# Kernel optimization log

Hardware: AMD Instinct MI355X
Metric: run time of the kernel (lower is better)

Reference implementation:

```python
import jax, jax.numpy as jnp
import numpy as np

NUM_ENTITIES = 100000
NUM_RELATIONS = 8
HIDDEN = 128
N_NODES = 100000
N_EDGES = 500000


def setup_inputs() -> dict:
    key = jax.random.key(0)
    ks = jax.random.split(key, 10)
    scale = 1.0 / np.sqrt(HIDDEN)
    inp = {
        "x_ids": jax.random.randint(ks[0], (N_NODES,), 0, NUM_ENTITIES),
        "edge_index": jax.random.randint(ks[1], (2, N_EDGES), 0, N_NODES),
        "edge_type": jax.random.randint(ks[2], (N_EDGES,), 0, NUM_RELATIONS),
        "emb": jax.random.normal(ks[3], (NUM_ENTITIES, HIDDEN), jnp.float32),
        "W1": jax.random.normal(ks[4], (NUM_RELATIONS, HIDDEN, HIDDEN), jnp.float32) * scale,
        "root1": jax.random.normal(ks[5], (HIDDEN, HIDDEN), jnp.float32) * scale,
        "b1": jnp.zeros((HIDDEN,), jnp.float32),
        "W2": jax.random.normal(ks[6], (NUM_RELATIONS, HIDDEN, HIDDEN), jnp.float32) * scale,
        "root2": jax.random.normal(ks[7], (HIDDEN, HIDDEN), jnp.float32) * scale,
        "b2": jnp.zeros((HIDDEN,), jnp.float32),
    }
    return inp


def rgcn_conv(x, edge_index, edge_type, W, root, bias):
    # x: [N, d]; W: [R, d, d]; PyG RGCNConv with aggr='mean' (per-relation mean)
    N, d = x.shape
    R = W.shape[0]
    src, dst = edge_index[0], edge_index[1]
    # transform every node under every relation: [N, R, d]
    h = jnp.einsum('nd,rdf->nrf', x, W)
    msg = h[src, edge_type]                       # [E, d] gather per edge
    seg = dst * R + edge_type                     # composite (node, relation) segment id
    sums = jax.ops.segment_sum(msg, seg, num_segments=N * R)
    cnt = jax.ops.segment_sum(jnp.ones((msg.shape[0], 1), x.dtype), seg, num_segments=N * R)
    agg = (sums / jnp.maximum(cnt, 1.0)).reshape(N, R, d).sum(axis=1)
    return agg + x @ root + bias


def reference(x_ids, edge_index, edge_type, emb, W1, root1, b1, W2, root2, b2):
    x = emb[x_ids]                                # embedding lookup [N, d]
    x = rgcn_conv(x, edge_index, edge_type, W1, root1, b1)
    x = jax.nn.relu(x)
    x = rgcn_conv(x, edge_index, edge_type, W2, root2, b2)
    return jax.nn.sigmoid(x)
```

## Files before the change

### kernel.cpp

```cpp
#include <hip/hip_runtime.h>

#define HD 128
#define RNUM 8
#define SCAN_BS 2048

typedef __attribute__((ext_vector_type(8))) short short8;
typedef __attribute__((ext_vector_type(4))) float float4e;

__device__ __forceinline__ unsigned short f2bf(float f) {
    unsigned int u = __float_as_uint(f);
    u += 0x7fffu + ((u >> 16) & 1u);
    return (unsigned short)(u >> 16);
}

__device__ __forceinline__ unsigned int pk2(float lo, float hi) {
    return (unsigned int)f2bf(lo) | ((unsigned int)f2bf(hi) << 16);
}

__device__ __forceinline__ void acc2(float4e& a, unsigned int u, int i) {
    a[i]     += __uint_as_float(u << 16);
    a[i + 1] += __uint_as_float(u & 0xffff0000u);
}

__device__ __forceinline__ void gload_lds16(const void* g, void* l) {
    __builtin_amdgcn_global_load_lds(
        (const __attribute__((address_space(1))) void*)g,
        (__attribute__((address_space(3))) void*)l, 16, 0, 0);
}

__global__ void zero_i(int* __restrict__ p, int n) {
    int g = blockIdx.x * blockDim.x + threadIdx.x;
    if (g < n) p[g] = 0;
}

__global__ void prep_kernel(const float* __restrict__ W1, const float* __restrict__ r1,
                            const float* __restrict__ W2, const float* __restrict__ r2,
                            unsigned short* __restrict__ WT,
                            const float* __restrict__ emb, unsigned short* __restrict__ emb16,
                            long long n8) {
    long long g = (long long)blockIdx.x * blockDim.x + threadIdx.x;
    if (g < 18 * 16384) {
        int gi = (int)g;
        int mat = gi >> 14;
        int idx = gi & 16383;
        int d = idx >> 7;
        int f = idx & 127;
        const float* src;
        int m;
        if (mat < 8)       { src = W1; m = mat; }
        else if (mat == 8) { src = r1; m = 0; }
        else if (mat < 17) { src = W2; m = mat - 9; }
        else               { src = r2; m = 0; }
        WT[mat * 16384 + f * 128 + d] = f2bf(src[(size_t)m * 16384 + d * 128 + f]);
    }
    long long h = g - 18 * 16384;
    if (h >= 0 && h < n8) {
        const float4* p = (const float4*)(emb + h * 8);
        float4 v0 = p[0], v1 = p[1];
        uint4 o;
        o.x = pk2(v0.x, v0.y);
        o.y = pk2(v0.z, v0.w);
        o.z = pk2(v1.x, v1.y);
        o.w = pk2(v1.z, v1.w);
        *(uint4*)(emb16 + h * 8) = o;
    }
}

__global__ void count_kernel(const int* __restrict__ ei, const int* __restrict__ et,
                             int* __restrict__ cnt, int E, int N) {
    int e = blockIdx.x * blockDim.x + threadIdx.x;
    if (e < E) atomicAdd(&cnt[ei[E + e] * RNUM + et[e]], 1);
}

__global__ void scan1(const int* __restrict__ in, int* __restrict__ out,
                      int* __restrict__ bsum, int n) {
    __shared__ int s[256];
    const int tid = threadIdx.x;
    const int base = blockIdx.x * SCAN_BS + tid * 8;
    int v[8];
    int sum = 0;
#pragma unroll
    for (int j = 0; j < 8; j++) {
        int x = (base + j < n) ? in[base + j] : 0;
        v[j] = sum;
        sum += x;
    }
    s[tid] = sum;
    __syncthreads();
    for (int off = 1; off < 256; off <<= 1) {
        int tv = (tid >= off) ? s[tid - off] : 0;
        __syncthreads();
        if (tid >= off) s[tid] += tv;
        __syncthreads();
    }
    int excl = (tid > 0) ? s[tid - 1] : 0;
    if (tid == 255) bsum[blockIdx.x] = s[255];
#pragma unroll
    for (int j = 0; j < 8; j++)
        if (base + j < n) out[base + j] = v[j] + excl;
}

__global__ void scan2(int* __restrict__ bsum, int nb) {
    __shared__ int s[512];
    const int tid = threadIdx.x;
    s[tid] = (tid < nb) ? bsum[tid] : 0;
    __syncthreads();
    for (int off = 1; off < 512; off <<= 1) {
        int tv = (tid >= off) ? s[tid - off] : 0;
        __syncthreads();
        if (tid >= off) s[tid] += tv;
        __syncthreads();
    }
    if (tid < nb) bsum[tid] = (tid > 0) ? s[tid - 1] : 0;
}

__global__ void scan3(int* __restrict__ out, int* __restrict__ cur,
                      const int* __restrict__ bsum, int n) {
    const int base = blockIdx.x * SCAN_BS + threadIdx.x * 8;
    const int add = bsum[blockIdx.x];
#pragma unroll
    for (int j = 0; j < 8; j++) {
        int i = base + j;
        if (i < n) {
            int v = out[i] + add;
            out[i] = v;
            cur[i] = v;
        }
    }
}

__global__ void fill_kernel(const int* __restrict__ ei, const int* __restrict__ et,
                            const int* __restrict__ ids,
                            int* __restrict__ cur, int* __restrict__ col,
                            int* __restrict__ colE, int* __restrict__ row_start,
                            int E, int N) {
    int e = blockIdx.x * blockDim.x + threadIdx.x;
    if (e == 0) row_start[RNUM * N] = E;
    if (e < E) {
        int src = ei[e];
        int pos = atomicAdd(&cur[ei[E + e] * RNUM + et[e]], 1);
        col[pos] = src;
        colE[pos] = ids[src];
    }
}

template <bool HAS_IDX, int ACT>
__launch_bounds__(256, 3)
__global__ void rgcn_fused(const int* __restrict__ row_start, const int* __restrict__ col,
                           const int* __restrict__ ids,
                           const unsigned short* __restrict__ x16,
                           const unsigned short* __restrict__ WT,
                           const float* __restrict__ bias,
                           void* __restrict__ CoutV, int N, int E) {
    __shared__ unsigned short As[64 * 128];
    __shared__ unsigned short Ws[128 * 128];

    const int tid = threadIdx.x;
    const int block0 = blockIdx.x * 64;
    const int w = tid >> 6;
    const int lane = tid & 63;
    const int ln15 = lane & 15;
    const int quad = lane >> 4;
    const int rowbase = (w & 1) * 32;
    const int colbase = (w >> 1) * 64;
    const int grp = tid >> 2;
    const int sub4 = tid & 3;
    const int mydst = block0 + grp;
    const bool rowok = (mydst < N);

    float4e acc[2][4];
#pragma unroll
    for (int i = 0; i < 2; i++)
#pragma unroll
        for (int j = 0; j < 4; j++)
#pragma unroll
            for (int q = 0; q < 4; q++) acc[i][j][q] = 0.0f;

#pragma unroll 1
    for (int s = 0; s < RNUM; s++) {
        {
            const unsigned short* Wsrc = WT + s * 16384;
#pragma unroll
            for (int i = 0; i < 8; i++) {
                int c = i * 256 + tid;
                int f = c >> 4;
                int cc = c & 15;
                const void* src = (const void*)(Wsrc + f * 128 + ((cc ^ (f & 15)) << 3));
                int cbase = i * 256 + (tid & ~63);
                gload_lds16(src, (char*)Ws + (size_t)cbase * 16);
            }
        }
        {
            float4e a[8];
#pragma unroll
            for (int j = 0; j < 8; j++) a[j] = (float4e){0.f, 0.f, 0.f, 0.f};
            int s0 = 0, s1 = 0;
            if (rowok) {
                s0 = row_start[mydst * 8 + s];
                s1 = row_start[mydst * 8 + s + 1];
            }
            const float inv = (s1 > s0) ? 1.0f / (float)(s1 - s0) : 0.0f;
            for (int e = s0; e < s1; e++) {
                int c = col[e];
                const uint4* xp = (const uint4*)(x16 + (size_t)c * HD + sub4 * 32);
                uint4 v0 = xp[0], v1 = xp[1], v2 = xp[2], v3 = xp[3];
                acc2(a[0], v0.x, 0); acc2(a[0], v0.y, 2);
                acc2(a[1], v0.z, 0); acc2(a[1], v0.w, 2);
                acc2(a[2], v1.x, 0); acc2(a[2], v1.y, 2);
                acc2(a[3], v1.z, 0); acc2(a[3], v1.w, 2);
                acc2(a[4], v2.x, 0); acc2(a[4], v2.y, 2);
                acc2(a[5], v2.z, 0); acc2(a[5], v2.w, 2);
                acc2(a[6], v3.x, 0); acc2(a[6], v3.y, 2);
                acc2(a[7], v3.z, 0); acc2(a[7], v3.w, 2);
            }
#pragma unroll
            for (int j = 0; j < 8; j++) a[j] *= inv;
#pragma unroll
            for (int j = 0; j < 4; j++) {
                uint4 o;
                o.x = pk2(a[2 * j][0], a[2 * j][1]);
                o.y = pk2(a[2 * j][2], a[2 * j][3]);
                o.z = pk2(a[2 * j + 1][0], a[2 * j + 1][1]);
                o.w = pk2(a[2 * j + 1][2], a[2 * j + 1][3]);
                int ck = sub4 * 4 + j;
                *(uint4*)&As[grp * 128 + ((ck ^ (grp & 15)) << 3)] = o;
            }
        }
        __syncthreads();

#pragma unroll
        for (int k0 = 0; k0 < 4; k0++) {
            short8 af[2], bf[4];
            const int ck = k0 * 4 + quad;
#pragma unroll
            for (int rt = 0; rt < 2; rt++) {
                int m = rowbase + rt * 16 + ln15;
                af[rt] = *(const short8*)&As[m * 128 + ((ck ^ (m & 15)) << 3)];
            }
#pragma unroll
            for (int ct = 0; ct < 4; ct++) {
                int n = colbase + ct * 16 + ln15;
                bf[ct] = *(const short8*)&Ws[n * 128 + ((ck ^ (n & 15)) << 3)];
            }
#pragma unroll
            for (int rt = 0; rt < 2; rt++)
#pragma unroll
                for (int ct = 0; ct < 4; ct++)
                    acc[rt][ct] = __builtin_amdgcn_mfma_f32_16x16x32_bf16(
                        af[rt], bf[ct], acc[rt][ct], 0, 0, 0);
        }
        __syncthreads();
    }

    {
        const unsigned short* Wsrc = WT + RNUM * 16384;
#pragma unroll
        for (int i = 0; i < 8; i++) {
            int c = i * 256 + tid;
            int f = c >> 4;
            int cc = c & 15;
            const void* src = (const void*)(Wsrc + f * 128 + ((cc ^ (f & 15)) << 3));
            int cbase = i * 256 + (tid & ~63);
            gload_lds16(src, (char*)Ws + (size_t)cbase * 16);
        }
        uint4 o0 = {0u, 0u, 0u, 0u}, o1 = o0, o2 = o0, o3 = o0;
        if (rowok) {
            int srcn = HAS_IDX ? ids[mydst] : mydst;
            const uint4* xp = (const uint4*)(x16 + (size_t)srcn * HD + sub4 * 32);
            o0 = xp[0]; o1 = xp[1]; o2 = xp[2]; o3 = xp[3];
        }
        const int ck0 = sub4 * 4;
        *(uint4*)&As[grp * 128 + (((ck0 + 0) ^ (grp & 15)) << 3)] = o0;
        *(uint4*)&As[grp * 128 + (((ck0 + 1) ^ (grp & 15)) << 3)] = o1;
        *(uint4*)&As[grp * 128 + (((ck0 + 2) ^ (grp & 15)) << 3)] = o2;
        *(uint4*)&As[grp * 128 + (((ck0 + 3) ^ (grp & 15)) << 3)] = o3;
        __syncthreads();
#pragma unroll
        for (int k0 = 0; k0 < 4; k0++) {
            short8 af[2], bf[4];
            const int ck = k0 * 4 + quad;
#pragma unroll
            for (int rt = 0; rt < 2; rt++) {
                int m = rowbase + rt * 16 + ln15;
                af[rt] = *(const short8*)&As[m * 128 + ((ck ^ (m & 15)) << 3)];
            }
#pragma unroll
            for (int ct = 0; ct < 4; ct++) {
                int n = colbase + ct * 16 + ln15;
                bf[ct] = *(const short8*)&Ws[n * 128 + ((ck ^ (n & 15)) << 3)];
            }
#pragma unroll
            for (int rt = 0; rt < 2; rt++)
#pragma unroll
                for (int ct = 0; ct < 4; ct++)
                    acc[rt][ct] = __builtin_amdgcn_mfma_f32_16x16x32_bf16(
                        af[rt], bf[ct], acc[rt][ct], 0, 0, 0);
        }
        __syncthreads();
    }

#pragma unroll
    for (int ct = 0; ct < 4; ct++) {
        int ncol = colbase + ct * 16 + ln15;
        float bv = bias[ncol];
#pragma unroll
        for (int rt = 0; rt < 2; rt++) {
#pragma unroll
            for (int rg = 0; rg < 4; rg++) {
                int rowg = block0 + rowbase + rt * 16 + quad * 4 + rg;
                if (rowg < N) {
                    float v = acc[rt][ct][rg] + bv;
                    if (ACT == 0) {
                        v = fmaxf(v, 0.0f);
                        ((unsigned short*)CoutV)[(size_t)rowg * HD + ncol] = f2bf(v);
                    } else {
                        v = 1.0f / (1.0f + expf(-v));
                        ((float*)CoutV)[(size_t)rowg * HD + ncol] = v;
                    }
                }
            }
        }
    }
}

extern "C" void kernel_launch(void* const* d_in, const int* in_sizes, int n_in,
                              void* d_out, int out_size, void* d_ws, size_t ws_size,
                              hipStream_t stream) {
    const int*   x_ids = (const int*)d_in[0];
    const int*   ei    = (const int*)d_in[1];
    const int*   et    = (const int*)d_in[2];
    const float* emb   = (const float*)d_in[3];
    const float* W1    = (const float*)d_in[4];
    const float* root1 = (const float*)d_in[5];
    const float* b1    = (const float*)d_in[6];
    const float* W2    = (const float*)d_in[7];
    const float* root2 = (const float*)d_in[8];
    const float* b2    = (const float*)d_in[9];

    const int N = in_sizes[0];
    const int E = in_sizes[1] / 2;
    const int NS = RNUM * N;
    const long long embElems = (long long)in_sizes[3];
    float* out = (float*)d_out;

    char* ws = (char*)d_ws;
    size_t off = 0;
    int* row_start = (int*)(ws + off); off += (size_t)(NS + 4) * 4;
    int* col       = (int*)(ws + off); off += (size_t)E * 4;
    int* colE      = (int*)(ws + off); off += (size_t)E * 4;
    int* bsum      = (int*)(ws + off); off += 4096;
    unsigned short* WT    = (unsigned short*)(ws + off); off += (size_t)18 * 16384 * 2;
    unsigned short* emb16 = (unsigned short*)(ws + off); off += (size_t)embElems * 2;
    unsigned short* z16   = (unsigned short*)(ws + off); off += (size_t)N * HD * 2;
    int* cur = (int*)z16;

    const int scanBlocks = (NS + SCAN_BS - 1) / SCAN_BS;
    const int layerGrid = (N + 63) / 64;

    zero_i<<<(NS + 255) / 256, 256, 0, stream>>>(cur, NS);
    count_kernel<<<(E + 255) / 256, 256, 0, stream>>>(ei, et, cur, E, N);
    scan1<<<scanBlocks, 256, 0, stream>>>(cur, row_start, bsum, NS);
    scan2<<<1, 512, 0, stream>>>(bsum, scanBlocks);
    scan3<<<scanBlocks, 256, 0, stream>>>(row_start, cur, bsum, NS);
    fill_kernel<<<(E + 255) / 256, 256, 0, stream>>>(ei, et, x_ids, cur, col, colE,
                                                     row_start, E, N);

    {
        long long n8 = embElems / 8;
        long long total = 18 * 16384 + n8;
        prep_kernel<<<(unsigned int)((total + 255) / 256), 256, 0, stream>>>(
            W1, root1, W2, root2, WT, emb, emb16, n8);
    }

    rgcn_fused<true, 0><<<layerGrid, 256, 0, stream>>>(
        row_start, colE, x_ids, emb16, WT, b1, (void*)z16, N, E);
    rgcn_fused<false, 1><<<layerGrid, 256, 0, stream>>>(
        row_start, col, nullptr, z16, WT + 9 * 16384, b2, (void*)out, N, E);
}
```

Baseline: 407.8 us.

## Hoist all relation gathers ahead of MFMA loop, use 512 threads per block

The fused RGCN kernel now runs 512 threads per block, with 8 threads per destination row instead of 4. Each thread first gathers and averages the neighbor features for all 8 relations and keeps them packed in registers. A single 9-step MFMA loop then consumes them, and the next relation's weight tile is loaded into LDS after each step's compute. This separates the irregular gather phase from the matrix phase, doubles gather parallelism per row and overlaps weight loads with the loop. The cost is higher register pressure from 16 uint4 values per thread, a smaller per-wave MFMA tile, and a tighter launch bound that may cause spills.

After: 504.8 us. 23.8% more time.

```diff
diff --git a/kernel.cpp b/kernel.cpp
--- a/kernel.cpp
+++ b/kernel.cpp
@@ -145,7 +145,7 @@
 }
 
 template <bool HAS_IDX, int ACT>
-__launch_bounds__(256, 3)
+__launch_bounds__(512, 4)
 __global__ void rgcn_fused(const int* __restrict__ row_start, const int* __restrict__ col,
                            const int* __restrict__ ids,
                            const unsigned short* __restrict__ x16,
@@ -162,145 +162,128 @@
     const int ln15 = lane & 15;
     const int quad = lane >> 4;
     const int rowbase = (w & 1) * 32;
-    const int colbase = (w >> 1) * 64;
-    const int grp = tid >> 2;
-    const int sub4 = tid & 3;
+    const int colbase = (w >> 1) * 32;
+    const int grp = tid >> 3;
+    const int sub8 = tid & 7;
     const int mydst = block0 + grp;
     const bool rowok = (mydst < N);
 
-    float4e acc[2][4];
+    {
+        const unsigned short* Wsrc = WT;
+#pragma unroll
+        for (int i = 0; i < 4; i++) {
+            int c = i * 512 + tid;
+            int f = c >> 4;
+            int cc = c & 15;
+            const void* src = (const void*)(Wsrc + f * 128 + ((cc ^ (f & 15)) << 3));
+            int cbase = i * 512 + (tid & ~63);
+            gload_lds16(src, (char*)Ws + (size_t)cbase * 16);
+        }
+    }
+
+    uint4 p[8][2];
+#pragma unroll
+    for (int r = 0; r < 8; r++) {
+        float4e a0 = {0.f, 0.f, 0.f, 0.f};
+        float4e a1 = {0.f, 0.f, 0.f, 0.f};
+        float4e a2 = {0.f, 0.f, 0.f, 0.f};
+        float4e a3 = {0.f, 0.f, 0.f, 0.f};
+        int s0 = 0, s1 = 0;
+        if (rowok) {
+            s0 = row_start[mydst * 8 + r];
+            s1 = row_start[mydst * 8 + r + 1];
+        }
+#pragma unroll 1
+        for (int e = s0; e < s1; e++) {
+            int c = col[e];
+            const uint4* xp = (const uint4*)(x16 + (size_t)c * HD + sub8 * 16);
+            uint4 v0 = xp[0], v1 = xp[1];
+            acc2(a0, v0.x, 0); acc2(a0, v0.y, 2);
+            acc2(a1, v0.z, 0); acc2(a1, v0.w, 2);
+            acc2(a2, v1.x, 0); acc2(a2, v1.y, 2);
+            acc2(a3, v1.z, 0); acc2(a3, v1.w, 2);
+        }
+        const float inv = (s1 > s0) ? 1.0f / (float)(s1 - s0) : 0.0f;
+        a0 *= inv; a1 *= inv; a2 *= inv; a3 *= inv;
+        p[r][0].x = pk2(a0[0], a0[1]);
+        p[r][0].y = pk2(a0[2], a0[3]);
+        p[r][0].z = pk2(a1[0], a1[1]);
+        p[r][0].w = pk2(a1[2], a1[3]);
+        p[r][1].x = pk2(a2[0], a2[1]);
+        p[r][1].y = pk2(a2[2], a2[3]);
+        p[r][1].z = pk2(a3[0], a3[1]);
+        p[r][1].w = pk2(a3[2], a3[3]);
+    }
+
+    float4e acc[2][2];
 #pragma unroll
     for (int i = 0; i < 2; i++)
 #pragma unroll
-        for (int j = 0; j < 4; j++)
+        for (int j = 0; j < 2; j++)
 #pragma unroll
             for (int q = 0; q < 4; q++) acc[i][j][q] = 0.0f;
 
-#pragma unroll 1
-    for (int s = 0; s < RNUM; s++) {
-        {
-            const unsigned short* Wsrc = WT + s * 16384;
-#pragma unroll
-            for (int i = 0; i < 8; i++) {
-                int c = i * 256 + tid;
+    const int ck0 = sub8 * 2;
+    const int wr0 = grp * 128 + ((ck0 ^ (grp & 15)) << 3);
+    const int wr1 = grp * 128 + (((ck0 + 1) ^ (grp & 15)) << 3);
+
+#pragma unroll
+    for (int s = 0; s < 9; s++) {
+        if (s < 8) {
+            *(uint4*)&As[wr0] = p[s][0];
+            *(uint4*)&As[wr1] = p[s][1];
+        } else {
+            uint4 r0 = {0u, 0u, 0u, 0u}, r1 = {0u, 0u, 0u, 0u};
+            if (rowok) {
+                int srcn = HAS_IDX ? ids[mydst] : mydst;
+                const uint4* xp = (const uint4*)(x16 + (size_t)srcn * HD + sub8 * 16);
+                r0 = xp[0];
+                r1 = xp[1];
+            }
+            *(uint4*)&As[wr0] = r0;
+            *(uint4*)&As[wr1] = r1;
+        }
+        __syncthreads();
+
+#pragma unroll
+        for (int k0 = 0; k0 < 4; k0++) {
+            short8 af[2], bf[2];
+            const int ck = k0 * 4 + quad;
+#pragma unroll
+            for (int rt = 0; rt < 2; rt++) {
+                int m = rowbase + rt * 16 + ln15;
+                af[rt] = *(const short8*)&As[m * 128 + ((ck ^ (m & 15)) << 3)];
+            }
+#pragma unroll
+            for (int ct = 0; ct < 2; ct++) {
+                int n = colbase + ct * 16 + ln15;
+                bf[ct] = *(const short8*)&Ws[n * 128 + ((ck ^ (n & 15)) << 3)];
+            }
+#pragma unroll
+            for (int rt = 0; rt < 2; rt++)
+#pragma unroll
+                for (int ct = 0; ct < 2; ct++)
+                    acc[rt][ct] = __builtin_amdgcn_mfma_f32_16x16x32_bf16(
+                        af[rt], bf[ct], acc[rt][ct], 0, 0, 0);
+        }
+        __syncthreads();
+
+        if (s < 8) {
+            const unsigned short* Wsrc = WT + (s + 1) * 16384;
+#pragma unroll
+            for (int i = 0; i < 4; i++) {
+                int c = i * 512 + tid;
                 int f = c >> 4;
                 int cc = c & 15;
                 const void* src = (const void*)(Wsrc + f * 128 + ((cc ^ (f & 15)) << 3));
-                int cbase = i * 256 + (tid & ~63);
+                int cbase = i * 512 + (tid & ~63);
                 gload_lds16(src, (char*)Ws + (size_t)cbase * 16);
             }
         }
-        {
-            float4e a[8];
-#pragma unroll
-            for (int j = 0; j < 8; j++) a[j] = (float4e){0.f, 0.f, 0.f, 0.f};
-            int s0 = 0, s1 = 0;
-            if (rowok) {
-                s0 = row_start[mydst * 8 + s];
-                s1 = row_start[mydst * 8 + s + 1];
-            }
-            const float inv = (s1 > s0) ? 1.0f / (float)(s1 - s0) : 0.0f;
-            for (int e = s0; e < s1; e++) {
-                int c = col[e];
-                const uint4* xp = (const uint4*)(x16 + (size_t)c * HD + sub4 * 32);
-                uint4 v0 = xp[0], v1 = xp[1], v2 = xp[2], v3 = xp[3];
-                acc2(a[0], v0.x, 0); acc2(a[0], v0.y, 2);
-                acc2(a[1], v0.z, 0); acc2(a[1], v0.w, 2);
-                acc2(a[2], v1.x, 0); acc2(a[2], v1.y, 2);
-                acc2(a[3], v1.z, 0); acc2(a[3], v1.w, 2);
-                acc2(a[4], v2.x, 0); acc2(a[4], v2.y, 2);
-                acc2(a[5], v2.z, 0); acc2(a[5], v2.w, 2);
-                acc2(a[6], v3.x, 0); acc2(a[6], v3.y, 2);
-                acc2(a[7], v3.z, 0); acc2(a[7], v3.w, 2);
-            }
-#pragma unroll
-            for (int j = 0; j < 8; j++) a[j] *= inv;
-#pragma unroll
-            for (int j = 0; j < 4; j++) {
-                uint4 o;
-                o.x = pk2(a[2 * j][0], a[2 * j][1]);
-                o.y = pk2(a[2 * j][2], a[2 * j][3]);
-                o.z = pk2(a[2 * j + 1][0], a[2 * j + 1][1]);
-                o.w = pk2(a[2 * j + 1][2], a[2 * j + 1][3]);
-                int ck = sub4 * 4 + j;
-                *(uint4*)&As[grp * 128 + ((ck ^ (grp & 15)) << 3)] = o;
-            }
-        }
-        __syncthreads();
-
-#pragma unroll
-        for (int k0 = 0; k0 < 4; k0++) {
-            short8 af[2], bf[4];
-            const int ck = k0 * 4 + quad;
-#pragma unroll
-            for (int rt = 0; rt < 2; rt++) {
-                int m = rowbase + rt * 16 + ln15;
-                af[rt] = *(const short8*)&As[m * 128 + ((ck ^ (m & 15)) << 3)];
-            }
-#pragma unroll
-            for (int ct = 0; ct < 4; ct++) {
-                int n = colbase + ct * 16 + ln15;
-                bf[ct] = *(const short8*)&Ws[n * 128 + ((ck ^ (n & 15)) << 3)];
-            }
-#pragma unroll
-            for (int rt = 0; rt < 2; rt++)
-#pragma unroll
-                for (int ct = 0; ct < 4; ct++)
-                    acc[rt][ct] = __builtin_amdgcn_mfma_f32_16x16x32_bf16(
-                        af[rt], bf[ct], acc[rt][ct], 0, 0, 0);
-        }
-        __syncthreads();
-    }
-
-    {
-        const unsigned short* Wsrc = WT + RNUM * 16384;
-#pragma unroll
-        for (int i = 0; i < 8; i++) {
-            int c = i * 256 + tid;
-            int f = c >> 4;
-            int cc = c & 15;
-            const void* src = (const void*)(Wsrc + f * 128 + ((cc ^ (f & 15)) << 3));
-            int cbase = i * 256 + (tid & ~63);
-            gload_lds16(src, (char*)Ws + (size_t)cbase * 16);
-        }
-        uint4 o0 = {0u, 0u, 0u, 0u}, o1 = o0, o2 = o0, o3 = o0;
-        if (rowok) {
-            int srcn = HAS_IDX ? ids[mydst] : mydst;
-            const uint4* xp = (const uint4*)(x16 + (size_t)srcn * HD + sub4 * 32);
-            o0 = xp[0]; o1 = xp[1]; o2 = xp[2]; o3 = xp[3];
-        }
-        const int ck0 = sub4 * 4;
-        *(uint4*)&As[grp * 128 + (((ck0 + 0) ^ (grp & 15)) << 3)] = o0;
-        *(uint4*)&As[grp * 128 + (((ck0 + 1) ^ (grp & 15)) << 3)] = o1;
-        *(uint4*)&As[grp * 128 + (((ck0 + 2) ^ (grp & 15)) << 3)] = o2;
-        *(uint4*)&As[grp * 128 + (((ck0 + 3) ^ (grp & 15)) << 3)] = o3;
-        __syncthreads();
-#pragma unroll
-        for (int k0 = 0; k0 < 4; k0++) {
-            short8 af[2], bf[4];
-            const int ck = k0 * 4 + quad;
-#pragma unroll
-            for (int rt = 0; rt < 2; rt++) {
-                int m = rowbase + rt * 16 + ln15;
-                af[rt] = *(const short8*)&As[m * 128 + ((ck ^ (m & 15)) << 3)];
-            }
-#pragma unroll
-            for (int ct = 0; ct < 4; ct++) {
-                int n = colbase + ct * 16 + ln15;
-                bf[ct] = *(const short8*)&Ws[n * 128 + ((ck ^ (n & 15)) << 3)];
-            }
-#pragma unroll
-            for (int rt = 0; rt < 2; rt++)
-#pragma unroll
-                for (int ct = 0; ct < 4; ct++)
-                    acc[rt][ct] = __builtin_amdgcn_mfma_f32_16x16x32_bf16(
-                        af[rt], bf[ct], acc[rt][ct], 0, 0, 0);
-        }
-        __syncthreads();
-    }
-
-#pragma unroll
-    for (int ct = 0; ct < 4; ct++) {
+    }
+
+#pragma unroll
+    for (int ct = 0; ct < 2; ct++) {
         int ncol = colbase + ct * 16 + ln15;
         float bv = bias[ncol];
 #pragma unroll
@@ -372,8 +355,8 @@
             W1, root1, W2, root2, WT, emb, emb16, n8);
     }
 
-    rgcn_fused<true, 0><<<layerGrid, 256, 0, stream>>>(
+    rgcn_fused<true, 0><<<layerGrid, 512, 0, stream>>>(
         row_start, colE, x_ids, emb16, WT, b1, (void*)z16, N, E);
-    rgcn_fused<false, 1><<<layerGrid, 256, 0, stream>>>(
+    rgcn_fused<false, 1><<<layerGrid, 512, 0, stream>>>(
         row_start, col, nullptr, z16, WT + 9 * 16384, b2, (void*)out, N, E);
 }
```
